# Optimization experiments

Measured on AMD Instinct MI355X. Metric: run time of the kernel, lower is better.

## Reference

```python
import jax, jax.numpy as jnp
import numpy as np

NUM_HEADS = 8


def _layernorm(x, w, b, eps=1e-5):
    # normalize over last axis (channels)
    mu = jnp.mean(x, axis=-1, keepdims=True)
    var = jnp.var(x, axis=-1, keepdims=True)
    return (x - mu) * jax.lax.rsqrt(var + eps) * w + b


def setup_inputs() -> dict:
    key = jax.random.key(0)
    ks = jax.random.split(key, 5)
    B, C, H, W = 8, 512, 32, 32
    x = jax.random.normal(ks[0], (B, C, H, W), dtype=jnp.float32)
    ln_w = jnp.ones((C,), dtype=jnp.float32)
    ln_b = jnp.zeros((C,), dtype=jnp.float32)
    qkv_w = jax.random.normal(ks[1], (3 * C, C), dtype=jnp.float32) * (1.0 / np.sqrt(C))
    qkv_b = jax.random.normal(ks[2], (3 * C,), dtype=jnp.float32) * 0.02
    proj_w = jax.random.normal(ks[3], (C, C), dtype=jnp.float32) * (1.0 / np.sqrt(C))
    proj_b = jax.random.normal(ks[4], (C,), dtype=jnp.float32) * 0.02
    return {"x": x, "ln_w": ln_w, "ln_b": ln_b, "qkv_w": qkv_w,
            "qkv_b": qkv_b, "proj_w": proj_w, "proj_b": proj_b}


def reference(x, ln_w, ln_b, qkv_w, qkv_b, proj_w, proj_b):
    B, C, H, W = x.shape
    nh = NUM_HEADS
    hd = C // nh
    HW = H * W
    residual = x
    # LayerNorm over channels: (B,C,H,W) -> (B,H,W,C)
    xn = _layernorm(x.transpose(0, 2, 3, 1), ln_w, ln_b)  # (B,H,W,C)
    # 1x1 conv == per-pixel linear: (B,H,W,3C)
    qkv = jnp.einsum('bhwc,oc->bhwo', xn, qkv_w) + qkv_b
    # match torch reshape (B,3,nh,hd,HW).permute(1,0,2,4,3)
    qkv = qkv.reshape(B, HW, 3, nh, hd).transpose(2, 0, 3, 1, 4)  # (3,B,nh,HW,hd)
    q, k, v = qkv[0], qkv[1], qkv[2]
    scale = 1.0 / jnp.sqrt(jnp.asarray(hd, dtype=x.dtype))
    attn = jnp.einsum('bnqd,bnkd->bnqk', q, k) * scale  # (B,nh,HW,HW)
    attn = jax.nn.softmax(attn, axis=-1)
    out = jnp.einsum('bnqk,bnkd->bnqd', attn, v)  # (B,nh,HW,hd)
    out = out.transpose(0, 2, 1, 3).reshape(B, H, W, C)
    out = jnp.einsum('bhwc,oc->bhwo', out, proj_w) + proj_b
    return out.transpose(0, 3, 1, 2) + residual
```

## Files before the change

### kernel.cpp

```cpp
#include <hip/hip_runtime.h>

typedef __bf16 bf16;
typedef __bf16 bf16x8 __attribute__((ext_vector_type(8)));
typedef float f32x4 __attribute__((ext_vector_type(4)));

#define MFMA16(a, b, c) __builtin_amdgcn_mfma_f32_16x16x32_bf16(a, b, c, 0, 0, 0)

#define QSCALE 0.1803368801111137f

#define BARRIER_ONLY() asm volatile("s_barrier" ::: "memory")
#define WAITVM_BARRIER(N) \
  asm volatile("s_waitcnt vmcnt(" #N ")\n\ts_barrier" ::: "memory")

static __device__ __forceinline__ unsigned int pack2(float a, float b) {
  unsigned short s0 = __builtin_bit_cast(unsigned short, (bf16)a);
  unsigned short s1 = __builtin_bit_cast(unsigned short, (bf16)b);
  return (unsigned int)s0 | ((unsigned int)s1 << 16);
}

static __device__ __forceinline__ void gl16(const bf16* g, bf16* l) {
  __builtin_amdgcn_global_load_lds(
      (const __attribute__((address_space(1))) unsigned int*)g,
      (__attribute__((address_space(3))) unsigned int*)l, 16, 0, 0);
}

__global__ __launch_bounds__(256) void convert_w(const float* __restrict__ qkvw,
                                                 const float* __restrict__ projw,
                                                 bf16* __restrict__ wc) {
  int c4 = blockIdx.x * 256 + threadIdx.x;
  const float* src = (c4 < 196608) ? (qkvw + (size_t)c4 * 4)
                                   : (projw + (size_t)(c4 - 196608) * 4);
  float4 v = *(const float4*)src;
  uint2 o;
  o.x = pack2(v.x, v.y);
  o.y = pack2(v.z, v.w);
  *(uint2*)&wc[(size_t)c4 * 4] = o;
}

__global__ __launch_bounds__(256) void ln_kernel(const float* __restrict__ x,
                                                 const float* __restrict__ lnw,
                                                 const float* __restrict__ lnb,
                                                 bf16* __restrict__ xn) {
  __shared__ float tile[512 * 17];
  __shared__ float wsh[512];
  __shared__ float bsh[512];
  const int t = threadIdx.x;
  const int b = blockIdx.x >> 6;
  const int p0 = (blockIdx.x & 63) * 16;
  for (int i = t; i < 512; i += 256) {
    wsh[i] = lnw[i];
    bsh[i] = lnb[i];
  }
  const float* xb = x + (size_t)b * 524288 + p0;
#pragma unroll
  for (int i = 0; i < 8; ++i) {
    int chunk = t + 256 * i;
    int c = chunk >> 2, px4 = (chunk & 3) * 4;
    float4 v = *(const float4*)&xb[(size_t)c * 1024 + px4];
    tile[c * 17 + px4 + 0] = v.x;
    tile[c * 17 + px4 + 1] = v.y;
    tile[c * 17 + px4 + 2] = v.z;
    tile[c * 17 + px4 + 3] = v.w;
  }
  __syncthreads();
  const int pix = t >> 4, j = t & 15;
  float sum = 0.f, sq = 0.f;
#pragma unroll
  for (int i = 0; i < 32; ++i) {
    int c = i * 16 + j;
    float v = tile[c * 17 + pix];
    sum += v;
    sq += v * v;
  }
#pragma unroll
  for (int m = 1; m <= 8; m <<= 1) {
    sum += __shfl_xor(sum, m);
    sq += __shfl_xor(sq, m);
  }
  float mu = sum * (1.f / 512.f);
  float var = sq * (1.f / 512.f) - mu * mu;
  float rstd = rsqrtf(var + 1e-5f);
  unsigned int* orow =
      (unsigned int*)(xn + ((size_t)(b * 1024 + p0 + pix)) * 512);
#pragma unroll
  for (int i = 0; i < 16; ++i) {
    int dw = i * 16 + j;
    int c0 = 2 * dw, c1 = 2 * dw + 1;
    float v0 = (tile[c0 * 17 + pix] - mu) * rstd * wsh[c0] + bsh[c0];
    float v1 = (tile[c1 * 17 + pix] - mu) * rstd * wsh[c1] + bsh[c1];
    orow[dw] = pack2(v0, v1);
  }
}

__global__ __launch_bounds__(256, 3) void gemm_qkv(
    const bf16* __restrict__ A, const bf16* __restrict__ Bm,
    const float* __restrict__ bias, bf16* __restrict__ oq,
    bf16* __restrict__ okk, bf16* __restrict__ ov) {
  __shared__ bf16 smem[16384];
  bf16* ash = smem;
  bf16* bsh = smem + 8192;
  const int t = threadIdx.x;
  const int lane = t & 63, w = t >> 6;
  const int quad = lane >> 4, r16 = lane & 15;
  const int wm = w >> 1, wn = w & 1;
  const int pid = blockIdx.x;
  const int panel = pid / 96, within = pid % 96;
  const int m0 = (panel * 8 + (within & 7)) * 128;
  const int n0 = (within >> 3) * 128;
  int soff[4];
  int sr[4];
#pragma unroll
  for (int j = 0; j < 4; ++j) {
    int c = (w * 4 + j) * 64 + lane;
    int r = c >> 3, cc = c & 7;
    sr[j] = r;
    soff[j] = (cc ^ (r & 7)) * 8;
  }
  f32x4 acc[4][4] = {};
  for (int k0 = 0; k0 < 512; k0 += 64) {
#pragma unroll
    for (int j = 0; j < 4; ++j) {
      gl16(&A[(size_t)(m0 + sr[j]) * 512 + k0 + soff[j]],
           &ash[(w * 4 + j) * 512]);
      gl16(&Bm[(size_t)(n0 + sr[j]) * 512 + k0 + soff[j]],
           &bsh[(w * 4 + j) * 512]);
    }
    __syncthreads();
#pragma unroll
    for (int kc = 0; kc < 2; ++kc) {
      bf16x8 af[4], bfr[4];
#pragma unroll
      for (int i = 0; i < 4; ++i) {
        int row = wm * 64 + i * 16 + r16;
        af[i] = *(const bf16x8*)&ash[row * 64 +
                                     ((kc * 4 + quad) ^ (r16 & 7)) * 8];
      }
#pragma unroll
      for (int i = 0; i < 4; ++i) {
        int row = wn * 64 + i * 16 + r16;
        bfr[i] = *(const bf16x8*)&bsh[row * 64 +
                                      ((kc * 4 + quad) ^ (r16 & 7)) * 8];
      }
#pragma unroll
      for (int tm = 0; tm < 4; ++tm)
#pragma unroll
        for (int tn = 0; tn < 4; ++tn)
          acc[tm][tn] = MFMA16(af[tm], bfr[tn], acc[tm][tn]);
    }
    __syncthreads();
  }
  if (n0 < 1024) {
#pragma unroll
    for (int tm = 0; tm < 4; ++tm) {
#pragma unroll
      for (int tn = 0; tn < 4; ++tn) {
        int n = n0 + wn * 64 + tn * 16 + r16;
        float bn = bias[n];
        int comp = n >> 9, h = (n >> 6) & 7, d = n & 63;
#pragma unroll
        for (int r = 0; r < 4; ++r) {
          int m = m0 + wm * 64 + tm * 16 + quad * 4 + r;
          float v = acc[tm][tn][r] + bn;
          int b = m >> 10, p = m & 1023;
          size_t base = ((size_t)(b * 8 + h)) * 65536;
          if (comp == 0)
            oq[base + (size_t)p * 64 + d] = (bf16)(v * QSCALE);
          else
            okk[base + (size_t)p * 64 + d] = (bf16)v;
        }
      }
    }
  } else {
    bf16* tb = &smem[w * 4096];
#pragma unroll
    for (int tn = 0; tn < 4; ++tn) {
      int n = n0 + wn * 64 + tn * 16 + r16;
      float bn = bias[n];
      int row = tn * 16 + r16;
#pragma unroll
      for (int tm = 0; tm < 4; ++tm) {
        f32x4 a = acc[tm][tn];
        uint2 pk;
        pk.x = pack2(a[0] + bn, a[1] + bn);
        pk.y = pack2(a[2] + bn, a[3] + bn);
        int g = (tm * 2 + (quad >> 1)) ^ (row & 7);
        *(uint2*)&tb[row * 64 + g * 8 + (quad & 1) * 4] = pk;
      }
    }
    const int h = ((n0 - 1024) >> 6) + wn;
    const int mw = m0 + wm * 64;
    const int b = mw >> 10;
    bf16* vbase = ov + ((size_t)(b * 8 + h)) * 65536 + (mw & 1023);
#pragma unroll
    for (int pass = 0; pass < 8; ++pass) {
      int row = pass * 8 + (lane >> 3);
      int g = (lane & 7) ^ (row & 7);
      uint4 vd = *(uint4*)&tb[row * 64 + g * 8];
      *(uint4*)&vbase[(size_t)row * 1024 + (lane & 7) * 8] = vd;
    }
  }
}

__global__ __launch_bounds__(256, 4) void gemm_proj(
    const bf16* __restrict__ Wm, const bf16* __restrict__ A,
    const float* __restrict__ bias, const float* __restrict__ resid,
    float* __restrict__ op) {
  __shared__ bf16 ash[2][4096];
  __shared__ bf16 bsh[2][4096];
  const int t = threadIdx.x;
  const int lane = t & 63, w = t >> 6;
  const int quad = lane >> 4, r16 = lane & 15;
  const int wm = w >> 1, wn = w & 1;
  const int m0 = blockIdx.x * 64, n0 = blockIdx.y * 64;
  int soff[2], sr[2];
#pragma unroll
  for (int j = 0; j < 2; ++j) {
    int c = (w * 2 + j) * 64 + lane;
    int r = c >> 3, cc = c & 7;
    sr[j] = r;
    soff[j] = (cc ^ (r & 7)) * 8;
  }
  f32x4 acc[2][2] = {};
  auto stage = [&](int k0, int buf) {
#pragma unroll
    for (int j = 0; j < 2; ++j) {
      gl16(&Wm[(size_t)(m0 + sr[j]) * 512 + k0 + soff[j]],
           &ash[buf][(w * 2 + j) * 512]);
      gl16(&A[(size_t)(n0 + sr[j]) * 512 + k0 + soff[j]],
           &bsh[buf][(w * 2 + j) * 512]);
    }
  };
  auto compute = [&](int buf) {
#pragma unroll
    for (int kc = 0; kc < 2; ++kc) {
      bf16x8 af[2], bfr[2];
#pragma unroll
      for (int i = 0; i < 2; ++i) {
        int row = wm * 32 + i * 16 + r16;
        af[i] = *(const bf16x8*)&ash[buf][row * 64 +
                                          ((kc * 4 + quad) ^ (r16 & 7)) * 8];
      }
#pragma unroll
      for (int i = 0; i < 2; ++i) {
        int row = wn * 32 + i * 16 + r16;
        bfr[i] = *(const bf16x8*)&bsh[buf][row * 64 +
                                           ((kc * 4 + quad) ^ (r16 & 7)) * 8];
      }
#pragma unroll
      for (int tm = 0; tm < 2; ++tm)
#pragma unroll
        for (int tn = 0; tn < 2; ++tn)
          acc[tm][tn] = MFMA16(af[tm], bfr[tn], acc[tm][tn]);
    }
  };
  stage(0, 0);
  for (int it = 0; it < 8; ++it) {
    const int cur = it & 1;
    if (it > 0) BARRIER_ONLY();
    if (it < 7) {
      stage((it + 1) * 64, cur ^ 1);
      WAITVM_BARRIER(4);
    } else {
      WAITVM_BARRIER(0);
    }
    compute(cur);
  }
#pragma unroll
  for (int tm = 0; tm < 2; ++tm) {
#pragma unroll
    for (int tn = 0; tn < 2; ++tn) {
      int n = n0 + wn * 32 + tn * 16 + r16;
      int b = n >> 10, p = n & 1023;
#pragma unroll
      for (int r = 0; r < 4; ++r) {
        int m = m0 + wm * 32 + tm * 16 + quad * 4 + r;
        size_t idx = ((size_t)(b * 512 + m)) * 1024 + p;
        op[idx] = acc[tm][tn][r] + bias[m] + resid[idx];
      }
    }
  }
}

__global__ __launch_bounds__(256, 4) void attn_kernel(
    const bf16* __restrict__ q, const bf16* __restrict__ k,
    const bf16* __restrict__ vT, bf16* __restrict__ o) {
  __shared__ bf16 kt[2][4096];
  __shared__ bf16 vt[2][4096];
  __shared__ bf16 psh[4][16 * 36];
  const int t = threadIdx.x;
  const int lane = t & 63, w = t >> 6;
  const int quad = lane >> 4, r16 = lane & 15;
  const int bh = blockIdx.x;
  const int qt0 = blockIdx.y * 64;
  const bf16* qb = q + (size_t)bh * 65536;
  const bf16* kb = k + (size_t)bh * 65536;
  const bf16* vb = vT + (size_t)bh * 65536;
  const int qrow = qt0 + w * 16 + r16;
  bf16x8 qf0 = *(const bf16x8*)&qb[(size_t)qrow * 64 + quad * 8];
  bf16x8 qf1 = *(const bf16x8*)&qb[(size_t)qrow * 64 + 32 + quad * 8];
  int offk[2], offv[2];
#pragma unroll
  for (int j = 0; j < 2; ++j) {
    int c = (w * 2 + j) * 64 + lane;
    int r = c >> 3, cc = c & 7;
    int sw = (cc ^ (r & 7)) * 8;
    offk[j] = r * 64 + sw;
    offv[j] = r * 1024 + sw;
  }
  f32x4 rsum = {};
  f32x4 oacc[4] = {};
  bf16* pw = psh[w];
  const int swz = r16 & 7;
  auto stage = [&](int tile, int buf) {
    size_t kv = (size_t)tile * 64;
#pragma unroll
    for (int j = 0; j < 2; ++j) {
      gl16(&kb[kv * 64 + offk[j]], &kt[buf][(w * 2 + j) * 512]);
      gl16(&vb[kv + offv[j]], &vt[buf][(w * 2 + j) * 512]);
    }
  };
  auto compute = [&](int buf) {
    const bf16* ktc = kt[buf];
    const bf16* vtc = vt[buf];
    f32x4 s[4];
#pragma unroll
    for (int tn = 0; tn < 4; ++tn) {
      const bf16* kr = &ktc[(tn * 16 + r16) * 64];
      bf16x8 kf0 = *(const bf16x8*)&kr[(quad ^ swz) * 8];
      bf16x8 kf1 = *(const bf16x8*)&kr[((4 + quad) ^ swz) * 8];
      f32x4 z = {};
      z = MFMA16(qf0, kf0, z);
      z = MFMA16(qf1, kf1, z);
      s[tn] = z;
    }
#pragma unroll
    for (int tn = 0; tn < 4; ++tn)
#pragma unroll
      for (int r = 0; r < 4; ++r) {
        float p = __builtin_exp2f(s[tn][r]);
        s[tn][r] = p;
        rsum[r] += p;
      }
#pragma unroll
    for (int kc = 0; kc < 2; ++kc) {
#pragma unroll
      for (int tt = 0; tt < 2; ++tt)
#pragma unroll
        for (int r = 0; r < 4; ++r)
          pw[(quad * 4 + r) * 36 + tt * 16 + r16] = (bf16)s[kc * 2 + tt][r];
      bf16x8 pf = *(const bf16x8*)&pw[r16 * 36 + quad * 8];
#pragma unroll
      for (int tn = 0; tn < 4; ++tn) {
        const bf16* vr = &vtc[(tn * 16 + r16) * 64];
        bf16x8 vf = *(const bf16x8*)&vr[((kc * 4 + quad) ^ swz) * 8];
        oacc[tn] = MFMA16(pf, vf, oacc[tn]);
      }
    }
  };
  stage(0, 0);
  for (int it = 0; it < 16; ++it) {
    const int cur = it & 1;
    if (it > 0) BARRIER_ONLY();
    if (it < 15) {
      stage(it + 1, cur ^ 1);
      WAITVM_BARRIER(4);
    } else {
      WAITVM_BARRIER(0);
    }
    compute(cur);
  }
#pragma unroll
  for (int msk = 1; msk <= 8; msk <<= 1)
#pragma unroll
    for (int r = 0; r < 4; ++r) rsum[r] += __shfl_xor(rsum[r], msk);
  float inv[4];
#pragma unroll
  for (int r = 0; r < 4; ++r) inv[r] = 1.f / rsum[r];
  const int b = bh >> 3, h = bh & 7;
#pragma unroll
  for (int tn = 0; tn < 4; ++tn)
#pragma unroll
    for (int r = 0; r < 4; ++r) {
      int p = qt0 + w * 16 + quad * 4 + r;
      o[((size_t)(b * 1024 + p)) * 512 + h * 64 + tn * 16 + r16] =
          (bf16)(oacc[tn][r] * inv[r]);
    }
}

extern "C" void kernel_launch(void* const* d_in, const int* in_sizes, int n_in,
                              void* d_out, int out_size, void* d_ws,
                              size_t ws_size, hipStream_t stream) {
  (void)in_sizes;
  (void)n_in;
  (void)out_size;
  (void)ws_size;
  const float* x = (const float*)d_in[0];
  const float* lnw = (const float*)d_in[1];
  const float* lnb = (const float*)d_in[2];
  const float* qkvw = (const float*)d_in[3];
  const float* qkvb = (const float*)d_in[4];
  const float* projw = (const float*)d_in[5];
  const float* projb = (const float*)d_in[6];
  float* out = (float*)d_out;

  const size_t NELEM = 4194304;
  bf16* wc = (bf16*)d_ws;
  bf16* xn = wc + 1048576;
  bf16* qws = xn + NELEM;
  bf16* kws = qws + NELEM;
  bf16* vws = kws + NELEM;
  bf16* aws = xn;

  convert_w<<<dim3(1024), dim3(256), 0, stream>>>(qkvw, projw, wc);
  ln_kernel<<<dim3(512), dim3(256), 0, stream>>>(x, lnw, lnb, xn);
  gemm_qkv<<<dim3(768), dim3(256), 0, stream>>>(xn, wc, qkvb, qws, kws, vws);
  attn_kernel<<<dim3(64, 16), dim3(256), 0, stream>>>(qws, kws, vws, aws);
  gemm_proj<<<dim3(8, 128), dim3(256), 0, stream>>>(wc + 786432, aws, projb, x,
                                                    out);
}
```

Measured before the change: 163.2 us.

## Process 32 query rows per wave in attention to reuse K/V tiles

Each wave in the attention kernel now handles two 16-row query fragments, so a block covers 128 queries and the grid shrinks from 16 to 8 query tiles per head. Each K/V tile staged into shared memory feeds twice as many MFMAs, which halves global K/V traffic and LDS fragment reads per query. The pipeline sync also changes from explicit vmcnt waits plus s_barrier to plain __syncthreads after compute. The cost is more registers (launch bounds lowered to 2), fewer blocks to fill the GPU, and possibly less overlap of loads with compute.

Result: no change. 164.1 us (+0.6%).

```diff
diff --git a/kernel.cpp b/kernel.cpp
--- a/kernel.cpp
+++ b/kernel.cpp
@@ -281,23 +281,27 @@
   }
 }
 
-__global__ __launch_bounds__(256, 4) void attn_kernel(
+__global__ __launch_bounds__(256, 2) void attn_kernel(
     const bf16* __restrict__ q, const bf16* __restrict__ k,
     const bf16* __restrict__ vT, bf16* __restrict__ o) {
   __shared__ bf16 kt[2][4096];
   __shared__ bf16 vt[2][4096];
-  __shared__ bf16 psh[4][16 * 36];
+  __shared__ bf16 psh[4][32 * 36];
   const int t = threadIdx.x;
   const int lane = t & 63, w = t >> 6;
   const int quad = lane >> 4, r16 = lane & 15;
   const int bh = blockIdx.x;
-  const int qt0 = blockIdx.y * 64;
+  const int qt0 = blockIdx.y * 128;
   const bf16* qb = q + (size_t)bh * 65536;
   const bf16* kb = k + (size_t)bh * 65536;
   const bf16* vb = vT + (size_t)bh * 65536;
-  const int qrow = qt0 + w * 16 + r16;
-  bf16x8 qf0 = *(const bf16x8*)&qb[(size_t)qrow * 64 + quad * 8];
-  bf16x8 qf1 = *(const bf16x8*)&qb[(size_t)qrow * 64 + 32 + quad * 8];
+  const int qrow = qt0 + w * 32 + r16;
+  bf16x8 qf0[2], qf1[2];
+#pragma unroll
+  for (int f = 0; f < 2; ++f) {
+    qf0[f] = *(const bf16x8*)&qb[(size_t)(qrow + f * 16) * 64 + quad * 8];
+    qf1[f] = *(const bf16x8*)&qb[(size_t)(qrow + f * 16) * 64 + 32 + quad * 8];
+  }
   int offk[2], offv[2];
 #pragma unroll
   for (int j = 0; j < 2; ++j) {
@@ -307,8 +311,8 @@
     offk[j] = r * 64 + sw;
     offv[j] = r * 1024 + sw;
   }
-  f32x4 rsum = {};
-  f32x4 oacc[4] = {};
+  f32x4 rsum[2] = {};
+  f32x4 oacc[2][4] = {};
   bf16* pw = psh[w];
   const int swz = r16 & 7;
   auto stage = [&](int tile, int buf) {
@@ -322,69 +326,80 @@
   auto compute = [&](int buf) {
     const bf16* ktc = kt[buf];
     const bf16* vtc = vt[buf];
-    f32x4 s[4];
+    f32x4 s[2][4];
 #pragma unroll
     for (int tn = 0; tn < 4; ++tn) {
       const bf16* kr = &ktc[(tn * 16 + r16) * 64];
       bf16x8 kf0 = *(const bf16x8*)&kr[(quad ^ swz) * 8];
       bf16x8 kf1 = *(const bf16x8*)&kr[((4 + quad) ^ swz) * 8];
-      f32x4 z = {};
-      z = MFMA16(qf0, kf0, z);
-      z = MFMA16(qf1, kf1, z);
-      s[tn] = z;
-    }
-#pragma unroll
-    for (int tn = 0; tn < 4; ++tn)
-#pragma unroll
-      for (int r = 0; r < 4; ++r) {
-        float p = __builtin_exp2f(s[tn][r]);
-        s[tn][r] = p;
-        rsum[r] += p;
-      }
+#pragma unroll
+      for (int f = 0; f < 2; ++f) {
+        f32x4 z = {};
+        z = MFMA16(qf0[f], kf0, z);
+        z = MFMA16(qf1[f], kf1, z);
+        s[f][tn] = z;
+      }
+    }
+#pragma unroll
+    for (int f = 0; f < 2; ++f)
+#pragma unroll
+      for (int tn = 0; tn < 4; ++tn)
+#pragma unroll
+        for (int r = 0; r < 4; ++r) {
+          float p = __builtin_exp2f(s[f][tn][r]);
+          s[f][tn][r] = p;
+          rsum[f][r] += p;
+        }
 #pragma unroll
     for (int kc = 0; kc < 2; ++kc) {
 #pragma unroll
-      for (int tt = 0; tt < 2; ++tt)
-#pragma unroll
-        for (int r = 0; r < 4; ++r)
-          pw[(quad * 4 + r) * 36 + tt * 16 + r16] = (bf16)s[kc * 2 + tt][r];
-      bf16x8 pf = *(const bf16x8*)&pw[r16 * 36 + quad * 8];
+      for (int f = 0; f < 2; ++f)
+#pragma unroll
+        for (int tt = 0; tt < 2; ++tt)
+#pragma unroll
+          for (int r = 0; r < 4; ++r)
+            pw[(f * 16 + quad * 4 + r) * 36 + tt * 16 + r16] =
+                (bf16)s[f][kc * 2 + tt][r];
+      bf16x8 pf0 = *(const bf16x8*)&pw[r16 * 36 + quad * 8];
+      bf16x8 pf1 = *(const bf16x8*)&pw[(16 + r16) * 36 + quad * 8];
 #pragma unroll
       for (int tn = 0; tn < 4; ++tn) {
         const bf16* vr = &vtc[(tn * 16 + r16) * 64];
         bf16x8 vf = *(const bf16x8*)&vr[((kc * 4 + quad) ^ swz) * 8];
-        oacc[tn] = MFMA16(pf, vf, oacc[tn]);
+        oacc[0][tn] = MFMA16(pf0, vf, oacc[0][tn]);
+        oacc[1][tn] = MFMA16(pf1, vf, oacc[1][tn]);
       }
     }
   };
   stage(0, 0);
+  __syncthreads();
   for (int it = 0; it < 16; ++it) {
     const int cur = it & 1;
-    if (it > 0) BARRIER_ONLY();
-    if (it < 15) {
-      stage(it + 1, cur ^ 1);
-      WAITVM_BARRIER(4);
-    } else {
-      WAITVM_BARRIER(0);
-    }
+    if (it < 15) stage(it + 1, cur ^ 1);
     compute(cur);
+    __syncthreads();
   }
 #pragma unroll
   for (int msk = 1; msk <= 8; msk <<= 1)
 #pragma unroll
-    for (int r = 0; r < 4; ++r) rsum[r] += __shfl_xor(rsum[r], msk);
-  float inv[4];
-#pragma unroll
-  for (int r = 0; r < 4; ++r) inv[r] = 1.f / rsum[r];
+    for (int f = 0; f < 2; ++f)
+#pragma unroll
+      for (int r = 0; r < 4; ++r) rsum[f][r] += __shfl_xor(rsum[f][r], msk);
   const int b = bh >> 3, h = bh & 7;
 #pragma unroll
-  for (int tn = 0; tn < 4; ++tn)
-#pragma unroll
-    for (int r = 0; r < 4; ++r) {
-      int p = qt0 + w * 16 + quad * 4 + r;
-      o[((size_t)(b * 1024 + p)) * 512 + h * 64 + tn * 16 + r16] =
-          (bf16)(oacc[tn][r] * inv[r]);
-    }
+  for (int f = 0; f < 2; ++f) {
+    float inv[4];
+#pragma unroll
+    for (int r = 0; r < 4; ++r) inv[r] = 1.f / rsum[f][r];
+#pragma unroll
+    for (int tn = 0; tn < 4; ++tn)
+#pragma unroll
+      for (int r = 0; r < 4; ++r) {
+        int p = qt0 + w * 32 + f * 16 + quad * 4 + r;
+        o[((size_t)(b * 1024 + p)) * 512 + h * 64 + tn * 16 + r16] =
+            (bf16)(oacc[f][tn][r] * inv[r]);
+      }
+  }
 }
 
 extern "C" void kernel_launch(void* const* d_in, const int* in_sizes, int n_in,
@@ -414,7 +429,7 @@
   convert_w<<<dim3(1024), dim3(256), 0, stream>>>(qkvw, projw, wc);
   ln_kernel<<<dim3(512), dim3(256), 0, stream>>>(x, lnw, lnb, xn);
   gemm_qkv<<<dim3(768), dim3(256), 0, stream>>>(xn, wc, qkvb, qws, kws, vws);
-  attn_kernel<<<dim3(64, 16), dim3(256), 0, stream>>>(qws, kws, vws, aws);
+  attn_kernel<<<dim3(64, 8), dim3(256), 0, stream>>>(qws, kws, vws, aws);
   gemm_proj<<<dim3(8, 128), dim3(256), 0, stream>>>(wc + 786432, aws, projb, x,
                                                     out);
 }
```

## Split attention QK^T by key rows across waves and share P through LDS

Applied to the files above, without the earlier changes.

In the attention kernel, each wave now computes scores for all 64 queries against its own 16-key slice, so it reads its K fragment once while holding all Q fragments in registers. The exp values go into one shared 64x72 P tile, which each wave then reads back by query rows for the PV MFMAs. Row sums are combined across waves through LDS at the end. The cost is an extra LDS barrier per tile, more registers for Q, and the lost min-blocks occupancy hint. The projection GEMM's pipeline is also simplified to a syncthreads-based double buffer.

Result: slower. 168.6 us (+3.3%).

```diff
diff --git a/kernel.cpp b/kernel.cpp
--- a/kernel.cpp
+++ b/kernel.cpp
@@ -8,7 +8,8 @@
 
 #define QSCALE 0.1803368801111137f
 
-#define BARRIER_ONLY() asm volatile("s_barrier" ::: "memory")
+#define LGKM_BARRIER() \
+  asm volatile("s_waitcnt lgkmcnt(0)\n\ts_barrier" ::: "memory")
 #define WAITVM_BARRIER(N) \
   asm volatile("s_waitcnt vmcnt(" #N ")\n\ts_barrier" ::: "memory")
 
@@ -254,16 +255,12 @@
     }
   };
   stage(0, 0);
+  __syncthreads();
   for (int it = 0; it < 8; ++it) {
     const int cur = it & 1;
-    if (it > 0) BARRIER_ONLY();
-    if (it < 7) {
-      stage((it + 1) * 64, cur ^ 1);
-      WAITVM_BARRIER(4);
-    } else {
-      WAITVM_BARRIER(0);
-    }
+    if (it < 7) stage((it + 1) * 64, cur ^ 1);
     compute(cur);
+    __syncthreads();
   }
 #pragma unroll
   for (int tm = 0; tm < 2; ++tm) {
@@ -281,12 +278,13 @@
   }
 }
 
-__global__ __launch_bounds__(256, 4) void attn_kernel(
-    const bf16* __restrict__ q, const bf16* __restrict__ k,
-    const bf16* __restrict__ vT, bf16* __restrict__ o) {
+__global__ __launch_bounds__(256) void attn_kernel(const bf16* __restrict__ q,
+                                                   const bf16* __restrict__ k,
+                                                   const bf16* __restrict__ vT,
+                                                   bf16* __restrict__ o) {
   __shared__ bf16 kt[2][4096];
   __shared__ bf16 vt[2][4096];
-  __shared__ bf16 psh[4][16 * 36];
+  __shared__ bf16 psh[64 * 72];
   const int t = threadIdx.x;
   const int lane = t & 63, w = t >> 6;
   const int quad = lane >> 4, r16 = lane & 15;
@@ -295,9 +293,13 @@
   const bf16* qb = q + (size_t)bh * 65536;
   const bf16* kb = k + (size_t)bh * 65536;
   const bf16* vb = vT + (size_t)bh * 65536;
-  const int qrow = qt0 + w * 16 + r16;
-  bf16x8 qf0 = *(const bf16x8*)&qb[(size_t)qrow * 64 + quad * 8];
-  bf16x8 qf1 = *(const bf16x8*)&qb[(size_t)qrow * 64 + 32 + quad * 8];
+  bf16x8 qa[4][2];
+#pragma unroll
+  for (int qt = 0; qt < 4; ++qt) {
+    const bf16* qr = &qb[(size_t)(qt0 + qt * 16 + r16) * 64];
+    qa[qt][0] = *(const bf16x8*)&qr[quad * 8];
+    qa[qt][1] = *(const bf16x8*)&qr[32 + quad * 8];
+  }
   int offk[2], offv[2];
 #pragma unroll
   for (int j = 0; j < 2; ++j) {
@@ -307,9 +309,8 @@
     offk[j] = r * 64 + sw;
     offv[j] = r * 1024 + sw;
   }
-  f32x4 rsum = {};
+  f32x4 rs[4] = {};
   f32x4 oacc[4] = {};
-  bf16* pw = psh[w];
   const int swz = r16 & 7;
   auto stage = [&](int tile, int buf) {
     size_t kv = (size_t)tile * 64;
@@ -319,63 +320,68 @@
       gl16(&vb[kv + offv[j]], &vt[buf][(w * 2 + j) * 512]);
     }
   };
-  auto compute = [&](int buf) {
-    const bf16* ktc = kt[buf];
-    const bf16* vtc = vt[buf];
+  stage(0, 0);
+  __syncthreads();
+  for (int it = 0; it < 16; ++it) {
+    const int cur = it & 1;
+    if (it < 15) stage(it + 1, cur ^ 1);
+    const bf16* ktc = kt[cur];
+    const bf16* vtc = vt[cur];
+    const bf16* kr = &ktc[(w * 16 + r16) * 64];
+    bf16x8 kf0 = *(const bf16x8*)&kr[(quad ^ swz) * 8];
+    bf16x8 kf1 = *(const bf16x8*)&kr[((4 + quad) ^ swz) * 8];
     f32x4 s[4];
 #pragma unroll
-    for (int tn = 0; tn < 4; ++tn) {
-      const bf16* kr = &ktc[(tn * 16 + r16) * 64];
-      bf16x8 kf0 = *(const bf16x8*)&kr[(quad ^ swz) * 8];
-      bf16x8 kf1 = *(const bf16x8*)&kr[((4 + quad) ^ swz) * 8];
+    for (int qt = 0; qt < 4; ++qt) {
       f32x4 z = {};
-      z = MFMA16(qf0, kf0, z);
-      z = MFMA16(qf1, kf1, z);
-      s[tn] = z;
-    }
-#pragma unroll
-    for (int tn = 0; tn < 4; ++tn)
+      z = MFMA16(qa[qt][0], kf0, z);
+      z = MFMA16(qa[qt][1], kf1, z);
+      s[qt] = z;
+    }
+#pragma unroll
+    for (int qt = 0; qt < 4; ++qt)
 #pragma unroll
       for (int r = 0; r < 4; ++r) {
-        float p = __builtin_exp2f(s[tn][r]);
-        s[tn][r] = p;
-        rsum[r] += p;
-      }
+        float p = __builtin_exp2f(s[qt][r]);
+        rs[qt][r] += p;
+        psh[(qt * 16 + quad * 4 + r) * 72 + w * 16 + r16] = (bf16)p;
+      }
+    LGKM_BARRIER();
 #pragma unroll
     for (int kc = 0; kc < 2; ++kc) {
-#pragma unroll
-      for (int tt = 0; tt < 2; ++tt)
-#pragma unroll
-        for (int r = 0; r < 4; ++r)
-          pw[(quad * 4 + r) * 36 + tt * 16 + r16] = (bf16)s[kc * 2 + tt][r];
-      bf16x8 pf = *(const bf16x8*)&pw[r16 * 36 + quad * 8];
+      bf16x8 af =
+          *(const bf16x8*)&psh[(w * 16 + r16) * 72 + kc * 32 + quad * 8];
 #pragma unroll
       for (int tn = 0; tn < 4; ++tn) {
         const bf16* vr = &vtc[(tn * 16 + r16) * 64];
         bf16x8 vf = *(const bf16x8*)&vr[((kc * 4 + quad) ^ swz) * 8];
-        oacc[tn] = MFMA16(pf, vf, oacc[tn]);
-      }
-    }
-  };
-  stage(0, 0);
-  for (int it = 0; it < 16; ++it) {
-    const int cur = it & 1;
-    if (it > 0) BARRIER_ONLY();
-    if (it < 15) {
-      stage(it + 1, cur ^ 1);
-      WAITVM_BARRIER(4);
-    } else {
-      WAITVM_BARRIER(0);
-    }
-    compute(cur);
+        oacc[tn] = MFMA16(af, vf, oacc[tn]);
+      }
+    }
+    WAITVM_BARRIER(0);
   }
 #pragma unroll
   for (int msk = 1; msk <= 8; msk <<= 1)
 #pragma unroll
-    for (int r = 0; r < 4; ++r) rsum[r] += __shfl_xor(rsum[r], msk);
+    for (int qt = 0; qt < 4; ++qt)
+#pragma unroll
+      for (int r = 0; r < 4; ++r) rs[qt][r] += __shfl_xor(rs[qt][r], msk);
+  float* rshf = (float*)psh;
+  if (r16 == 0) {
+#pragma unroll
+    for (int qt = 0; qt < 4; ++qt)
+#pragma unroll
+      for (int r = 0; r < 4; ++r)
+        rshf[w * 64 + qt * 16 + quad * 4 + r] = rs[qt][r];
+  }
+  __syncthreads();
   float inv[4];
 #pragma unroll
-  for (int r = 0; r < 4; ++r) inv[r] = 1.f / rsum[r];
+  for (int r = 0; r < 4; ++r) {
+    int ql = w * 16 + quad * 4 + r;
+    inv[r] = 1.f / (rshf[ql] + rshf[64 + ql] + rshf[128 + ql] +
+                    rshf[192 + ql]);
+  }
   const int b = bh >> 3, h = bh & 7;
 #pragma unroll
   for (int tn = 0; tn < 4; ++tn)
```
